# Optimization experiments

Measured on AMD Instinct MI355X. Metric: run time of the kernel, lower is better.

Reference implementation:

```python
import jax, jax.numpy as jnp
import numpy as np


def setup_inputs() -> dict:
    key = jax.random.key(0)
    kx, ky = jax.random.split(key)
    N, M, D = 16384, 16384, 512
    x = jax.random.normal(kx, (N, D), dtype=jnp.float32)
    y = jax.random.normal(ky, (M, D), dtype=jnp.float32)
    return {"x": x, "y": y, "device": 0}


def reference(x, y, device):
    # torch.cdist(x, y, p=2): pairwise Euclidean distances [N, M]
    # matching torch's large-matrix cdist path), clamped for numerical safety.
    x_sq = jnp.sum(x * x, axis=1, keepdims=True)          # [N, 1]
    y_sq = jnp.sum(y * y, axis=1)                          # [M]
    sq_dists = x_sq + y_sq[None, :] - 2.0 * (x @ y.T)      # [N, M]
    dists = jnp.sqrt(jnp.maximum(sq_dists, 0.0))
    # min over centers (dim=1), then argmax over candidates (dim=0)
    min_dists = jnp.min(dists, axis=1)                     # [N]
    max_id = jnp.argmax(min_dists)
    max_val = min_dists[max_id]
    return max_val, max_id
```

## Files before the change

### kernel.cpp

```cpp
#include <hip/hip_runtime.h>
#include <hip/hip_fp8.h>
#include <math.h>

#define N_ROWS 16384
#define M_ROWS 16384
#define DIM    512
#define JS     8
#define KCAND  256
#define DELTA  0.40f

typedef __attribute__((ext_vector_type(8))) int   int8v;
typedef __attribute__((ext_vector_type(4))) int   int4v;
typedef __attribute__((ext_vector_type(4))) float floatx4;

__global__ __launch_bounds__(256) void convert_kernel(const float* __restrict__ x, const float* __restrict__ y,
                                                      unsigned char* __restrict__ xh8, unsigned char* __restrict__ yh8,
                                                      float* __restrict__ x_sq, float* __restrict__ y_sq,
                                                      unsigned int* __restrict__ gmax_bits,
                                                      unsigned int* __restrict__ cnt, int* __restrict__ cand) {
    if (blockIdx.x == 0) {
        if (threadIdx.x < KCAND) cand[threadIdx.x] = 0;
        if (threadIdx.x == 0) { *gmax_bits = 0u; *cnt = 0u; }
    }
    int wave = threadIdx.x >> 6, lane = threadIdx.x & 63;
    int row = blockIdx.x * 4 + wave;
    const float* src; unsigned char* dst8; float* dsq; int r;
    if (row < N_ROWS) { r = row;          src = x; dst8 = xh8; dsq = x_sq; }
    else              { r = row - N_ROWS; src = y; dst8 = yh8; dsq = y_sq; }
    const float4* s4 = (const float4*)(src + (size_t)r * DIM);
    float4 a = s4[lane * 2];
    float4 b = s4[lane * 2 + 1];
    float v[8] = {a.x, a.y, a.z, a.w, b.x, b.y, b.z, b.w};
    union { unsigned char b[8]; uint2 u2; } pk;
    float s = 0.f;
    #pragma unroll
    for (int i = 0; i < 8; ++i) {
        s += v[i] * v[i];
        __hip_fp8_e4m3 q(v[i]);
        pk.b[i] = (unsigned char)q.__x;
    }
    *(uint2*)(dst8 + (size_t)r * DIM + lane * 8) = pk.u2;
    #pragma unroll
    for (int off = 32; off > 0; off >>= 1) s += __shfl_down(s, off, 64);
    if (lane == 0) dsq[r] = s;
}

__global__ __launch_bounds__(256, 2) void pass1_kernel(const unsigned char* __restrict__ xh8,
                                                       const unsigned char* __restrict__ yh8,
                                                       const float* __restrict__ y_sq,
                                                       float* __restrict__ part) {
    __shared__ __align__(16) unsigned char Bs[4][16384];
    __shared__ __align__(16) float ysq_s[M_ROWS / JS];
    __shared__ float red[4][64];

    const int t = threadIdx.x;
    const int w = t >> 6, lane = t & 63;
    const int col = lane & 15, q = lane >> 4;

    const int bid = blockIdx.x;
    const int wg = (bid & 7) * 256 + (bid >> 3);
    const int js = wg >> 8;
    const int i0 = (wg & 255) * 64;
    const int jbase = js * (M_ROWS / JS);

    {
        const float4* ys4 = (const float4*)(y_sq + jbase);
        float4 v0 = ys4[t * 2];
        float4 v1 = ys4[t * 2 + 1];
        *(float4*)&ysq_s[t * 8]     = v0;
        *(float4*)&ysq_s[t * 8 + 4] = v1;
    }

    int8v afr[4][4];
    {
        const unsigned char* ab = xh8 + (size_t)(i0 + col) * DIM + q * 32;
        #pragma unroll
        for (int mt = 0; mt < 4; ++mt)
            #pragma unroll
            for (int kc = 0; kc < 4; ++kc) {
                const int4v* p = (const int4v*)(ab + mt * 16 * DIM + kc * 128);
                int4v a0 = p[0], a1 = p[1];
                int8v f;
                f[0] = a0[0]; f[1] = a0[1]; f[2] = a0[2]; f[3] = a0[3];
                f[4] = a1[0]; f[5] = a1[1]; f[6] = a1[2]; f[7] = a1[3];
                afr[mt][kc] = f;
            }
    }

    const unsigned char* sp[4];
    {
        const unsigned char* tb = yh8 + (size_t)jbase * DIM;
        #pragma unroll
        for (int i = 0; i < 4; ++i) {
            int s  = w * 256 + i * 64 + lane;
            int g  = s >> 7, u = s & 127;
            int jl = (g << 4) + (u & 15);
            int c  = (u >> 4) ^ (u & 7);
            sp[i] = tb + jl * DIM + c * 16;
        }
    }
    const int Klane = col * 16 + (((q << 1) ^ (col & 7)) << 8);

    float minv[16];
    #pragma unroll
    for (int i = 0; i < 16; ++i) minv[i] = __builtin_inff();

    __syncthreads();

#define STAGE(BUF, TOFF)                                                                     \
    { _Pragma("unroll")                                                                      \
      for (int i_ = 0; i_ < 4; ++i_) {                                                       \
          __builtin_amdgcn_global_load_lds(                                                  \
              (const __attribute__((address_space(1))) void*)(sp[i_] + (TOFF)),              \
              (__attribute__((address_space(3))) void*)(&Bs[BUF][w * 4096 + i_ * 1024]),     \
              16, 0, 0);                                                                     \
      } }

    STAGE(0, 0)
    STAGE(1, 128)

    for (int jt = 0; jt < 16; ++jt) {
        floatx4 acc[4][2];
        #pragma unroll
        for (int mt = 0; mt < 4; ++mt) {
            acc[mt][0] = (floatx4){0.f, 0.f, 0.f, 0.f};
            acc[mt][1] = (floatx4){0.f, 0.f, 0.f, 0.f};
        }
        #pragma unroll
        for (int kc = 0; kc < 4; ++kc) {
            const int toff = (jt + (kc >> 1)) * (128 * DIM) + (((kc + 2) & 3) << 7);
            STAGE((kc + 2) & 3, toff)
            asm volatile("s_waitcnt vmcnt(8)" ::: "memory");
            __builtin_amdgcn_s_barrier();
            asm volatile("" ::: "memory");
            #pragma unroll
            for (int nt = 0; nt < 2; ++nt) {
                const unsigned char* gb = &Bs[kc][(w * 2 + nt) * 2048];
                int4v lo = *(const int4v*)(gb + Klane);
                int4v hi = *(const int4v*)(gb + (Klane ^ 256));
                int8v b;
                b[0] = lo[0]; b[1] = lo[1]; b[2] = lo[2]; b[3] = lo[3];
                b[4] = hi[0]; b[5] = hi[1]; b[6] = hi[2]; b[7] = hi[3];
                __builtin_amdgcn_s_setprio(1);
                #pragma unroll
                for (int mt = 0; mt < 4; ++mt)
                    acc[mt][nt] = __builtin_amdgcn_mfma_scale_f32_16x16x128_f8f6f4(
                        afr[mt][kc], b, acc[mt][nt],
                        0, 0,
                        0, 127,
                        0, 127);
                __builtin_amdgcn_s_setprio(0);
            }
        }
        #pragma unroll
        for (int nt = 0; nt < 2; ++nt) {
            float qv = ysq_s[jt * 128 + w * 32 + nt * 16 + col];
            #pragma unroll
            for (int mt = 0; mt < 4; ++mt)
                #pragma unroll
                for (int r = 0; r < 4; ++r)
                    minv[mt * 4 + r] = fminf(minv[mt * 4 + r], qv - 2.f * acc[mt][nt][r]);
        }
    }
#undef STAGE

    #pragma unroll
    for (int i = 0; i < 16; ++i) {
        float v = minv[i];
        v = fminf(v, __shfl_xor(v, 1, 64));
        v = fminf(v, __shfl_xor(v, 2, 64));
        v = fminf(v, __shfl_xor(v, 4, 64));
        v = fminf(v, __shfl_xor(v, 8, 64));
        minv[i] = v;
    }
    if (col == 0) {
        #pragma unroll
        for (int mt = 0; mt < 4; ++mt)
            #pragma unroll
            for (int r = 0; r < 4; ++r)
                red[w][mt * 16 + q * 4 + r] = minv[mt * 4 + r];
    }
    __syncthreads();
    if (t < 64)
        part[(size_t)(i0 + t) * JS + js] =
            fminf(fminf(red[0][t], red[1][t]), fminf(red[2][t], red[3][t]));
}

__global__ __launch_bounds__(1024) void maxred_kernel(const float* __restrict__ part,
                                                      const float* __restrict__ x_sq,
                                                      float* __restrict__ aval,
                                                      unsigned int* __restrict__ gmax_bits) {
    __shared__ float sm[1024];
    int t = threadIdx.x;
    int row = blockIdx.x * 1024 + t;
    float m = part[(size_t)row * JS];
    #pragma unroll
    for (int c = 1; c < JS; ++c) m = fminf(m, part[(size_t)row * JS + c]);
    float v = sqrtf(fmaxf(x_sq[row] + m, 0.f));
    aval[row] = v;
    sm[t] = v;
    __syncthreads();
    for (int s = 512; s > 0; s >>= 1) {
        if (t < s) sm[t] = fmaxf(sm[t], sm[t + s]);
        __syncthreads();
    }
    if (t == 0) atomicMax(gmax_bits, __float_as_uint(sm[0]));
}

__global__ __launch_bounds__(1024) void select_kernel(const float* __restrict__ aval,
                                                      const unsigned int* __restrict__ gmax_bits,
                                                      unsigned int* __restrict__ cnt,
                                                      int* __restrict__ cand) {
    int row = blockIdx.x * 1024 + threadIdx.x;
    float gmax = __uint_as_float(*gmax_bits);
    if (aval[row] >= gmax - DELTA) {
        unsigned s = atomicAdd(cnt, 1u);
        if (s < KCAND) cand[s] = row;
    }
}

#define TIr 64
#define LDA 68
#define LDB 132
__global__ __launch_bounds__(256) void rescore_kernel(const float* __restrict__ x, const float* __restrict__ y,
                                                      const float* __restrict__ y_sq,
                                                      const int* __restrict__ cand,
                                                      const unsigned int* __restrict__ cnt,
                                                      float* __restrict__ part2) {
    __shared__ __align__(16) float As[32 * LDA];
    __shared__ __align__(16) float Bs[32 * LDB];
    __shared__ float red[TIr][17];

    int t = threadIdx.x;
    int tx = t & 15, ty = t >> 4;
    int i0 = blockIdx.x * TIr;
    int j0 = blockIdx.y * 128;

    if ((unsigned)i0 >= *cnt) return;

    float acc[4][8];
    #pragma unroll
    for (int c = 0; c < 4; ++c)
        #pragma unroll
        for (int d = 0; d < 8; ++d) acc[c][d] = 0.f;

    int srow = t >> 3;
    int skq = (t & 7) * 4;
    int grow0 = cand[i0 + srow];
    int grow1 = cand[i0 + 32 + srow];

    for (int kc = 0; kc < DIM; kc += 32) {
        {
            float4 v = *(const float4*)(x + (size_t)grow0 * DIM + kc + skq);
            As[(skq + 0) * LDA + srow] = v.x;
            As[(skq + 1) * LDA + srow] = v.y;
            As[(skq + 2) * LDA + srow] = v.z;
            As[(skq + 3) * LDA + srow] = v.w;
            v = *(const float4*)(x + (size_t)grow1 * DIM + kc + skq);
            As[(skq + 0) * LDA + 32 + srow] = v.x;
            As[(skq + 1) * LDA + 32 + srow] = v.y;
            As[(skq + 2) * LDA + 32 + srow] = v.z;
            As[(skq + 3) * LDA + 32 + srow] = v.w;
        }
        #pragma unroll
        for (int it = 0; it < 4; ++it) {
            int row = it * 32 + srow;
            float4 v = *(const float4*)(y + (size_t)(j0 + row) * DIM + kc + skq);
            Bs[(skq + 0) * LDB + row] = v.x;
            Bs[(skq + 1) * LDB + row] = v.y;
            Bs[(skq + 2) * LDB + row] = v.z;
            Bs[(skq + 3) * LDB + row] = v.w;
        }
        __syncthreads();
        #pragma unroll 8
        for (int k = 0; k < 32; ++k) {
            float4 a  = *(const float4*)&As[k * LDA + ty * 4];
            float4 b0 = *(const float4*)&Bs[k * LDB + tx * 8];
            float4 b1 = *(const float4*)&Bs[k * LDB + tx * 8 + 4];
            float av[4] = {a.x, a.y, a.z, a.w};
            float bv[8] = {b0.x, b0.y, b0.z, b0.w, b1.x, b1.y, b1.z, b1.w};
            #pragma unroll
            for (int c = 0; c < 4; ++c)
                #pragma unroll
                for (int d = 0; d < 8; ++d)
                    acc[c][d] = fmaf(av[c], bv[d], acc[c][d]);
        }
        __syncthreads();
    }

    float4 q0 = *(const float4*)(y_sq + j0 + tx * 8);
    float4 q1 = *(const float4*)(y_sq + j0 + tx * 8 + 4);
    float qv[8] = {q0.x, q0.y, q0.z, q0.w, q1.x, q1.y, q1.z, q1.w};
    float mv[4] = {__builtin_inff(), __builtin_inff(), __builtin_inff(), __builtin_inff()};
    #pragma unroll
    for (int c = 0; c < 4; ++c)
        #pragma unroll
        for (int d = 0; d < 8; ++d)
            mv[c] = fminf(mv[c], qv[d] - 2.f * acc[c][d]);
    #pragma unroll
    for (int c = 0; c < 4; ++c) red[ty * 4 + c][tx] = mv[c];
    __syncthreads();
    if (t < TIr) {
        float m = red[t][0];
        #pragma unroll
        for (int xx = 1; xx < 16; ++xx) m = fminf(m, red[t][xx]);
        part2[(size_t)(i0 + t) * 128 + blockIdx.y] = m;
    }
}

__global__ __launch_bounds__(256) void final2_kernel(const float* __restrict__ part2,
                                                     const float* __restrict__ x_sq,
                                                     const int* __restrict__ cand,
                                                     const unsigned int* __restrict__ cnt,
                                                     float* __restrict__ out) {
    __shared__ float sv[256];
    __shared__ int si[256];
    int t = threadIdx.x;
    const float4* p4 = (const float4*)(part2 + (size_t)t * 128);
    float m = __builtin_inff();
    for (int c = 0; c < 32; ++c) {
        float4 v = p4[c];
        m = fminf(m, fminf(fminf(v.x, v.y), fminf(v.z, v.w)));
    }
    unsigned n = *cnt;
    if (n > KCAND) n = KCAND;
    int row = cand[t];
    float v = (t < (int)n) ? sqrtf(fmaxf(x_sq[row] + m, 0.f)) : -__builtin_inff();
    sv[t] = v; si[t] = row;
    __syncthreads();
    for (int s = 128; s > 0; s >>= 1) {
        if (t < s) {
            float v2 = sv[t + s]; int i2 = si[t + s];
            if (v2 > sv[t] || (v2 == sv[t] && i2 < si[t])) { sv[t] = v2; si[t] = i2; }
        }
        __syncthreads();
    }
    if (t == 0) { out[0] = sv[0]; out[1] = (float)si[0]; }
}

extern "C" void kernel_launch(void* const* d_in, const int* in_sizes, int n_in,
                              void* d_out, int out_size, void* d_ws, size_t ws_size,
                              hipStream_t stream) {
    const float* x = (const float*)d_in[0];
    const float* y = (const float*)d_in[1];
    float* out = (float*)d_out;

    char* w = (char*)d_ws;
    unsigned char* xh8 = (unsigned char*)w;
    unsigned char* yh8 = (unsigned char*)(w + (size_t)8388608);
    float* x_sq = (float*)(w + (size_t)16777216);
    float* y_sq = x_sq + N_ROWS;
    float* part = y_sq + M_ROWS;
    float* aval = part + (size_t)N_ROWS * JS;
    float* part2 = aval + N_ROWS;
    int* cand = (int*)(part2 + KCAND * 128);
    unsigned int* gmax_bits = (unsigned int*)(cand + KCAND);
    unsigned int* cnt = gmax_bits + 1;

    convert_kernel<<<(N_ROWS + M_ROWS) / 4, 256, 0, stream>>>(x, y, xh8, yh8, x_sq, y_sq, gmax_bits, cnt, cand);
    pass1_kernel<<<2048, 256, 0, stream>>>(xh8, yh8, y_sq, part);
    maxred_kernel<<<N_ROWS / 1024, 1024, 0, stream>>>(part, x_sq, aval, gmax_bits);
    select_kernel<<<N_ROWS / 1024, 1024, 0, stream>>>(aval, gmax_bits, cnt, cand);
    dim3 g2(KCAND / TIr, M_ROWS / 128);
    rescore_kernel<<<g2, 256, 0, stream>>>(x, y, y_sq, cand, cnt, part2);
    final2_kernel<<<1, 256, 0, stream>>>(part2, x_sq, cand, cnt, out);
}
```

Before: 321.4 us.

## Double row tile per block and split rows across waves in pass1

The pass1 block tile grows from 64 to 128 x-rows, and the grid halves to 1024 blocks. Each wave now owns 32 distinct rows across all 128 y-columns of a tile, so the cross-wave min reduction becomes a plain copy. The A fragments are staged through LDS with swizzled global_load_lds instead of direct per-lane global loads. The goal is to halve how often each block re-reads the y tiles and to cut redundant B-fragment reuse overhead, at the cost of fewer blocks (lower occupancy and wave count) and more LDS B reads per wave.

```diff
diff --git a/kernel.cpp b/kernel.cpp
--- a/kernel.cpp
+++ b/kernel.cpp
@@ -51,16 +51,16 @@
                                                        float* __restrict__ part) {
     __shared__ __align__(16) unsigned char Bs[4][16384];
     __shared__ __align__(16) float ysq_s[M_ROWS / JS];
-    __shared__ float red[4][64];
+    __shared__ float red[4][32];
 
     const int t = threadIdx.x;
     const int w = t >> 6, lane = t & 63;
     const int col = lane & 15, q = lane >> 4;
 
     const int bid = blockIdx.x;
-    const int wg = (bid & 7) * 256 + (bid >> 3);
-    const int js = wg >> 8;
-    const int i0 = (wg & 255) * 64;
+    const int wg = (bid & 7) * 128 + (bid >> 3);
+    const int js = wg >> 7;
+    const int i0 = (wg & 127) * 128;
     const int jbase = js * (M_ROWS / JS);
 
     {
@@ -71,47 +71,67 @@
         *(float4*)&ysq_s[t * 8 + 4] = v1;
     }
 
-    int8v afr[4][4];
     {
-        const unsigned char* ab = xh8 + (size_t)(i0 + col) * DIM + q * 32;
-        #pragma unroll
-        for (int mt = 0; mt < 4; ++mt)
+        const unsigned char* gs = xh8 + (size_t)i0 * DIM;
+        unsigned char* ls = (unsigned char*)Bs;
+        #pragma unroll
+        for (int it = 0; it < 16; ++it) {
+            int s  = it * 256 + t;
+            int r  = s >> 5;
+            int u  = s & 31;
+            int kq = u >> 3;
+            int cl = (u & 7) ^ (r & 7);
+            __builtin_amdgcn_global_load_lds(
+                (const __attribute__((address_space(1))) void*)(gs + r * 512 + kq * 128 + cl * 16),
+                (__attribute__((address_space(3))) void*)(ls + it * 4096 + w * 1024),
+                16, 0, 0);
+        }
+    }
+    __syncthreads();
+
+    int8v afr[2][4];
+    {
+        const unsigned char* ab = (const unsigned char*)Bs;
+        #pragma unroll
+        for (int mt = 0; mt < 2; ++mt) {
+            int rr = w * 32 + mt * 16 + col;
             #pragma unroll
             for (int kc = 0; kc < 4; ++kc) {
-                const int4v* p = (const int4v*)(ab + mt * 16 * DIM + kc * 128);
-                int4v a0 = p[0], a1 = p[1];
+                int base = rr * 512 + kc * 128 + (((q << 1) ^ (rr & 7)) << 4);
+                int4v a0 = *(const int4v*)(ab + base);
+                int4v a1 = *(const int4v*)(ab + (base ^ 16));
                 int8v f;
                 f[0] = a0[0]; f[1] = a0[1]; f[2] = a0[2]; f[3] = a0[3];
                 f[4] = a1[0]; f[5] = a1[1]; f[6] = a1[2]; f[7] = a1[3];
                 afr[mt][kc] = f;
             }
-    }
-
-    const unsigned char* sp[4];
+        }
+    }
+    __syncthreads();
+
+    int spo[4];
     {
-        const unsigned char* tb = yh8 + (size_t)jbase * DIM;
         #pragma unroll
         for (int i = 0; i < 4; ++i) {
             int s  = w * 256 + i * 64 + lane;
             int g  = s >> 7, u = s & 127;
             int jl = (g << 4) + (u & 15);
             int c  = (u >> 4) ^ (u & 7);
-            sp[i] = tb + jl * DIM + c * 16;
-        }
-    }
+            spo[i] = jl * DIM + c * 16;
+        }
+    }
+    const unsigned char* tb = yh8 + (size_t)jbase * DIM;
     const int Klane = col * 16 + (((q << 1) ^ (col & 7)) << 8);
 
-    float minv[16];
-    #pragma unroll
-    for (int i = 0; i < 16; ++i) minv[i] = __builtin_inff();
-
-    __syncthreads();
+    float minv[8];
+    #pragma unroll
+    for (int i = 0; i < 8; ++i) minv[i] = __builtin_inff();
 
 #define STAGE(BUF, TOFF)                                                                     \
     { _Pragma("unroll")                                                                      \
       for (int i_ = 0; i_ < 4; ++i_) {                                                       \
           __builtin_amdgcn_global_load_lds(                                                  \
-              (const __attribute__((address_space(1))) void*)(sp[i_] + (TOFF)),              \
+              (const __attribute__((address_space(1))) void*)(tb + spo[i_] + (TOFF)),        \
               (__attribute__((address_space(3))) void*)(&Bs[BUF][w * 4096 + i_ * 1024]),     \
               16, 0, 0);                                                                     \
       } }
@@ -120,12 +140,11 @@
     STAGE(1, 128)
 
     for (int jt = 0; jt < 16; ++jt) {
-        floatx4 acc[4][2];
-        #pragma unroll
-        for (int mt = 0; mt < 4; ++mt) {
-            acc[mt][0] = (floatx4){0.f, 0.f, 0.f, 0.f};
-            acc[mt][1] = (floatx4){0.f, 0.f, 0.f, 0.f};
-        }
+        floatx4 acc[2][8];
+        #pragma unroll
+        for (int mt = 0; mt < 2; ++mt)
+            #pragma unroll
+            for (int nt = 0; nt < 8; ++nt) acc[mt][nt] = (floatx4){0.f, 0.f, 0.f, 0.f};
         #pragma unroll
         for (int kc = 0; kc < 4; ++kc) {
             const int toff = (jt + (kc >> 1)) * (128 * DIM) + (((kc + 2) & 3) << 7);
@@ -134,29 +153,26 @@
             __builtin_amdgcn_s_barrier();
             asm volatile("" ::: "memory");
             #pragma unroll
-            for (int nt = 0; nt < 2; ++nt) {
-                const unsigned char* gb = &Bs[kc][(w * 2 + nt) * 2048];
+            for (int nt = 0; nt < 8; ++nt) {
+                const unsigned char* gb = &Bs[kc][nt * 2048];
                 int4v lo = *(const int4v*)(gb + Klane);
                 int4v hi = *(const int4v*)(gb + (Klane ^ 256));
                 int8v b;
                 b[0] = lo[0]; b[1] = lo[1]; b[2] = lo[2]; b[3] = lo[3];
                 b[4] = hi[0]; b[5] = hi[1]; b[6] = hi[2]; b[7] = hi[3];
                 __builtin_amdgcn_s_setprio(1);
-                #pragma unroll
-                for (int mt = 0; mt < 4; ++mt)
-                    acc[mt][nt] = __builtin_amdgcn_mfma_scale_f32_16x16x128_f8f6f4(
-                        afr[mt][kc], b, acc[mt][nt],
-                        0, 0,
-                        0, 127,
-                        0, 127);
+                acc[0][nt] = __builtin_amdgcn_mfma_scale_f32_16x16x128_f8f6f4(
+                    afr[0][kc], b, acc[0][nt], 0, 0, 0, 127, 0, 127);
+                acc[1][nt] = __builtin_amdgcn_mfma_scale_f32_16x16x128_f8f6f4(
+                    afr[1][kc], b, acc[1][nt], 0, 0, 0, 127, 0, 127);
                 __builtin_amdgcn_s_setprio(0);
             }
         }
         #pragma unroll
-        for (int nt = 0; nt < 2; ++nt) {
-            float qv = ysq_s[jt * 128 + w * 32 + nt * 16 + col];
-            #pragma unroll
-            for (int mt = 0; mt < 4; ++mt)
+        for (int nt = 0; nt < 8; ++nt) {
+            float qv = ysq_s[jt * 128 + nt * 16 + col];
+            #pragma unroll
+            for (int mt = 0; mt < 2; ++mt)
                 #pragma unroll
                 for (int r = 0; r < 4; ++r)
                     minv[mt * 4 + r] = fminf(minv[mt * 4 + r], qv - 2.f * acc[mt][nt][r]);
@@ -165,7 +181,7 @@
 #undef STAGE
 
     #pragma unroll
-    for (int i = 0; i < 16; ++i) {
+    for (int i = 0; i < 8; ++i) {
         float v = minv[i];
         v = fminf(v, __shfl_xor(v, 1, 64));
         v = fminf(v, __shfl_xor(v, 2, 64));
@@ -175,15 +191,14 @@
     }
     if (col == 0) {
         #pragma unroll
-        for (int mt = 0; mt < 4; ++mt)
+        for (int mt = 0; mt < 2; ++mt)
             #pragma unroll
             for (int r = 0; r < 4; ++r)
                 red[w][mt * 16 + q * 4 + r] = minv[mt * 4 + r];
     }
     __syncthreads();
-    if (t < 64)
-        part[(size_t)(i0 + t) * JS + js] =
-            fminf(fminf(red[0][t], red[1][t]), fminf(red[2][t], red[3][t]));
+    if (t < 128)
+        part[(size_t)(i0 + t) * JS + js] = red[t >> 5][t & 31];
 }
 
 __global__ __launch_bounds__(1024) void maxred_kernel(const float* __restrict__ part,
@@ -358,7 +373,7 @@
     unsigned int* cnt = gmax_bits + 1;
 
     convert_kernel<<<(N_ROWS + M_ROWS) / 4, 256, 0, stream>>>(x, y, xh8, yh8, x_sq, y_sq, gmax_bits, cnt, cand);
-    pass1_kernel<<<2048, 256, 0, stream>>>(xh8, yh8, y_sq, part);
+    pass1_kernel<<<1024, 256, 0, stream>>>(xh8, yh8, y_sq, part);
     maxred_kernel<<<N_ROWS / 1024, 1024, 0, stream>>>(part, x_sq, aval, gmax_bits);
     select_kernel<<<N_ROWS / 1024, 1024, 0, stream>>>(aval, gmax_bits, cnt, cand);
     dim3 g2(KCAND / TIr, M_ROWS / 128);
```

Measured after the change: 276.2 us. 14.1% less time.

## Double pass1 workgroup to 512 threads sharing staged B tiles across two row halves

Applied to the files above, without the earlier changes.

The pass1 kernel now uses 512-thread workgroups covering 128 x-rows instead of 64. Two groups of four waves share each staged y tile in LDS, which halves the global-to-LDS traffic for B per output row and halves the per-thread staging loads. The A fragments are now loaded through LDS with swizzled global_load_lds rather than direct global reads. The cost is larger workgroups, fewer blocks per CU in flight and an extra barrier phase at startup. The prefetch offset is also wrapped to stay in bounds.

```diff
diff --git a/kernel.cpp b/kernel.cpp
--- a/kernel.cpp
+++ b/kernel.cpp
@@ -45,74 +45,92 @@
     if (lane == 0) dsq[r] = s;
 }
 
-__global__ __launch_bounds__(256, 2) void pass1_kernel(const unsigned char* __restrict__ xh8,
+__global__ __launch_bounds__(512, 2) void pass1_kernel(const unsigned char* __restrict__ xh8,
                                                        const unsigned char* __restrict__ yh8,
                                                        const float* __restrict__ y_sq,
                                                        float* __restrict__ part) {
     __shared__ __align__(16) unsigned char Bs[4][16384];
     __shared__ __align__(16) float ysq_s[M_ROWS / JS];
-    __shared__ float red[4][64];
+    __shared__ float red[4][128];
 
     const int t = threadIdx.x;
     const int w = t >> 6, lane = t & 63;
     const int col = lane & 15, q = lane >> 4;
+    const int h = w >> 2, c = w & 3;
 
     const int bid = blockIdx.x;
-    const int wg = (bid & 7) * 256 + (bid >> 3);
-    const int js = wg >> 8;
-    const int i0 = (wg & 255) * 64;
+    const int wg = (bid & 7) * 128 + (bid >> 3);
+    const int js = wg >> 7;
+    const int i0 = (wg & 127) * 128;
     const int jbase = js * (M_ROWS / JS);
 
     {
         const float4* ys4 = (const float4*)(y_sq + jbase);
-        float4 v0 = ys4[t * 2];
-        float4 v1 = ys4[t * 2 + 1];
-        *(float4*)&ysq_s[t * 8]     = v0;
-        *(float4*)&ysq_s[t * 8 + 4] = v1;
-    }
+        *(float4*)&ysq_s[t * 4] = ys4[t];
+    }
+
+    {
+        const unsigned char* gs = xh8 + (size_t)i0 * DIM;
+        unsigned char* ls = (unsigned char*)Bs;
+        #pragma unroll
+        for (int it = 0; it < 8; ++it) {
+            int s  = it * 512 + t;
+            int r  = s >> 5;
+            int u  = s & 31;
+            int kq = u >> 3;
+            int cl = (u & 7) ^ (r & 7);
+            __builtin_amdgcn_global_load_lds(
+                (const __attribute__((address_space(1))) void*)(gs + r * 512 + kq * 128 + cl * 16),
+                (__attribute__((address_space(3))) void*)(ls + it * 8192 + w * 1024),
+                16, 0, 0);
+        }
+    }
+    __syncthreads();
 
     int8v afr[4][4];
     {
-        const unsigned char* ab = xh8 + (size_t)(i0 + col) * DIM + q * 32;
-        #pragma unroll
-        for (int mt = 0; mt < 4; ++mt)
+        const unsigned char* ab = (const unsigned char*)Bs;
+        #pragma unroll
+        for (int mt = 0; mt < 4; ++mt) {
+            int rr = h * 64 + mt * 16 + col;
             #pragma unroll
             for (int kc = 0; kc < 4; ++kc) {
-                const int4v* p = (const int4v*)(ab + mt * 16 * DIM + kc * 128);
-                int4v a0 = p[0], a1 = p[1];
+                int base = rr * 512 + kc * 128 + (((q << 1) ^ (rr & 7)) << 4);
+                int4v a0 = *(const int4v*)(ab + base);
+                int4v a1 = *(const int4v*)(ab + (base ^ 16));
                 int8v f;
                 f[0] = a0[0]; f[1] = a0[1]; f[2] = a0[2]; f[3] = a0[3];
                 f[4] = a1[0]; f[5] = a1[1]; f[6] = a1[2]; f[7] = a1[3];
                 afr[mt][kc] = f;
             }
-    }
-
-    const unsigned char* sp[4];
+        }
+    }
+    __syncthreads();
+
+    int spo[2];
     {
-        const unsigned char* tb = yh8 + (size_t)jbase * DIM;
-        #pragma unroll
-        for (int i = 0; i < 4; ++i) {
-            int s  = w * 256 + i * 64 + lane;
+        #pragma unroll
+        for (int i = 0; i < 2; ++i) {
+            int s  = i * 512 + t;
             int g  = s >> 7, u = s & 127;
             int jl = (g << 4) + (u & 15);
-            int c  = (u >> 4) ^ (u & 7);
-            sp[i] = tb + jl * DIM + c * 16;
-        }
-    }
+            int c2 = (u >> 4) ^ (u & 7);
+            spo[i] = jl * DIM + c2 * 16;
+        }
+    }
+    const unsigned char* tb = yh8 + (size_t)jbase * DIM;
     const int Klane = col * 16 + (((q << 1) ^ (col & 7)) << 8);
 
     float minv[16];
     #pragma unroll
     for (int i = 0; i < 16; ++i) minv[i] = __builtin_inff();
-
-    __syncthreads();
 
 #define STAGE(BUF, TOFF)                                                                     \
     { _Pragma("unroll")                                                                      \
-      for (int i_ = 0; i_ < 4; ++i_) {                                                       \
+      for (int i_ = 0; i_ < 2; ++i_) {                                                       \
           __builtin_amdgcn_global_load_lds(                                                  \
-              (const __attribute__((address_space(1))) void*)(sp[i_] + (TOFF)),              \
-              (__attribute__((address_space(3))) void*)(&Bs[BUF][w * 4096 + i_ * 1024]),     \
+              (const __attribute__((address_space(1))) void*)(tb + spo[i_] + (TOFF)),        \
+              (__attribute__((address_space(3))) void*)(&Bs[BUF][i_ * 8192 + w * 1024]),     \
               16, 0, 0);                                                                     \
       } }
 
@@ -128,14 +146,15 @@
         }
         #pragma unroll
         for (int kc = 0; kc < 4; ++kc) {
-            const int toff = (jt + (kc >> 1)) * (128 * DIM) + (((kc + 2) & 3) << 7);
+            const int jtp  = (jt + (kc >> 1)) & 15;
+            const int toff = jtp * (128 * DIM) + (((kc + 2) & 3) << 7);
             STAGE((kc + 2) & 3, toff)
-            asm volatile("s_waitcnt vmcnt(8)" ::: "memory");
+            asm volatile("s_waitcnt vmcnt(4)" ::: "memory");
             __builtin_amdgcn_s_barrier();
             asm volatile("" ::: "memory");
             #pragma unroll
             for (int nt = 0; nt < 2; ++nt) {
-                const unsigned char* gb = &Bs[kc][(w * 2 + nt) * 2048];
+                const unsigned char* gb = &Bs[kc][(c * 2 + nt) * 2048];
                 int4v lo = *(const int4v*)(gb + Klane);
                 int4v hi = *(const int4v*)(gb + (Klane ^ 256));
                 int8v b;
@@ -145,16 +164,13 @@
                 #pragma unroll
                 for (int mt = 0; mt < 4; ++mt)
                     acc[mt][nt] = __builtin_amdgcn_mfma_scale_f32_16x16x128_f8f6f4(
-                        afr[mt][kc], b, acc[mt][nt],
-                        0, 0,
-                        0, 127,
-                        0, 127);
+                        afr[mt][kc], b, acc[mt][nt], 0, 0, 0, 127, 0, 127);
                 __builtin_amdgcn_s_setprio(0);
             }
         }
         #pragma unroll
         for (int nt = 0; nt < 2; ++nt) {
-            float qv = ysq_s[jt * 128 + w * 32 + nt * 16 + col];
+            float qv = ysq_s[jt * 128 + c * 32 + nt * 16 + col];
             #pragma unroll
             for (int mt = 0; mt < 4; ++mt)
                 #pragma unroll
@@ -178,10 +194,10 @@
         for (int mt = 0; mt < 4; ++mt)
             #pragma unroll
             for (int r = 0; r < 4; ++r)
-                red[w][mt * 16 + q * 4 + r] = minv[mt * 4 + r];
-    }
-    __syncthreads();
-    if (t < 64)
+                red[c][h * 64 + mt * 16 + q * 4 + r] = minv[mt * 4 + r];
+    }
+    __syncthreads();
+    if (t < 128)
         part[(size_t)(i0 + t) * JS + js] =
             fminf(fminf(red[0][t], red[1][t]), fminf(red[2][t], red[3][t]));
 }
@@ -358,7 +374,7 @@
     unsigned int* cnt = gmax_bits + 1;
 
     convert_kernel<<<(N_ROWS + M_ROWS) / 4, 256, 0, stream>>>(x, y, xh8, yh8, x_sq, y_sq, gmax_bits, cnt, cand);
-    pass1_kernel<<<2048, 256, 0, stream>>>(xh8, yh8, y_sq, part);
+    pass1_kernel<<<1024, 512, 0, stream>>>(xh8, yh8, y_sq, part);
     maxred_kernel<<<N_ROWS / 1024, 1024, 0, stream>>>(part, x_sq, aval, gmax_bits);
     select_kernel<<<N_ROWS / 1024, 1024, 0, stream>>>(aval, gmax_bits, cnt, cand);
     dim3 g2(KCAND / TIr, M_ROWS / 128);
```

Result: faster. 285.4 us (-11.2%).
